# Kernel optimization log

Hardware: AMD Instinct MI355X
Metric: run time of the kernel (lower is better)

## Reference

```python
import jax, jax.numpy as jnp
import numpy as np

D = 1024
F = 256
EPS = 1e-5


def layer_norm(x, g, b):
    mu = jnp.mean(x, axis=-1, keepdims=True)
    var = jnp.mean((x - mu) ** 2, axis=-1, keepdims=True)
    return (x - mu) * jax.lax.rsqrt(var + EPS) * g + b


def setup_inputs() -> dict:
    key = jax.random.key(0)
    ks = jax.random.split(key, 8)
    B, S = 4, 4096
    return {
        "bottom_up_input": jax.random.normal(ks[0], (B, S, D), dtype=jnp.float32),
        "top_down_prediction": jax.random.normal(ks[1], (B, S, D), dtype=jnp.float32),
        "W_spec": jax.random.normal(ks[2], (2 * F, D), dtype=jnp.float32) * 0.02,
        "log_decay": jnp.linspace(-3.0, -0.001, F, dtype=jnp.float32),
        "frequencies": jax.random.normal(ks[3], (F,), dtype=jnp.float32) * 0.1,
        "W_from": jax.random.normal(ks[4], (D, 2 * F), dtype=jnp.float32) * 0.02,
        "ln1_g": jnp.ones((D,), jnp.float32),
        "ln1_b": jnp.zeros((D,), jnp.float32),
        "W1": jax.random.normal(ks[5], (D, D), dtype=jnp.float32) * 0.02,
        "b1": jnp.zeros((D,), jnp.float32),
        "W2": jax.random.normal(ks[6], (D, D), dtype=jnp.float32) * 0.02,
        "b2": jnp.zeros((D,), jnp.float32),
        "ln2_g": jnp.ones((D,), jnp.float32),
        "ln2_b": jnp.zeros((D,), jnp.float32),
        "error_weight": jnp.asarray(0.1, jnp.float32),
    }


def spectral_conv(x, W_spec, log_decay, frequencies, W_from, ln1_g, ln1_b):
    # x: [B,S,D]
    x = layer_norm(x, ln1_g, ln1_b)
    B, S, _ = x.shape
    spectral = jnp.einsum('bsd,fd->bsf', x, W_spec)  # [B,S,2F]
    u = jax.lax.complex(spectral[..., :F], spectral[..., F:])  # [B,S,F] complex
    decay = jax.nn.sigmoid(log_decay)
    omega = jnp.tanh(frequencies) * 0.1  # dt = 1.0
    rot = jax.lax.complex(jnp.cos(omega), jnp.sin(omega))  # [F]
    A = (decay * rot).astype(jnp.complex64)  # [F]
    # kernel[t] = A^t * rot, built with cumprod as in the original
    ones = jnp.ones((1, F), dtype=A.dtype)
    A_seq = jnp.broadcast_to(A[None, :], (S - 1, F))
    powers = jnp.cumprod(jnp.concatenate([ones, A_seq], axis=0), axis=0)  # [S,F]
    kernel = (powers * rot[None, :])[None]  # [1,S,F]
    n_fft = 2 * S
    U_f = jnp.fft.fft(u, n=n_fft, axis=1)
    K_f = jnp.fft.fft(kernel, n=n_fft, axis=1)
    y = jnp.fft.ifft(U_f * K_f, n=n_fft, axis=1)[:, :S, :]  # [B,S,F]
    spectral_out = jnp.concatenate([y.real, y.imag], axis=-1)  # [B,S,2F]
    return jnp.einsum('bsf,df->bsd', spectral_out, W_from)


def reference(bottom_up_input, top_down_prediction, W_spec, log_decay, frequencies,
              W_from, ln1_g, ln1_b, W1, b1, W2, b2, ln2_g, ln2_b, error_weight):
    bu_repr = spectral_conv(bottom_up_input, W_spec, log_decay, frequencies,
                            W_from, ln1_g, ln1_b)
    error = jnp.clip(bu_repr - top_down_prediction, -1.0, 1.0)
    corrected = bu_repr - jax.nn.sigmoid(error_weight) * error
    prediction_error = jnp.clip(jnp.mean(error ** 2), 0.0, 1.0)
    h = jax.nn.gelu(jnp.einsum('bsd,ed->bse', corrected, W1) + b1, approximate=False)
    h = jnp.einsum('bsd,ed->bse', h, W2) + b2
    next_prediction = layer_norm(h, ln2_g, ln2_b)
    return corrected, next_prediction, prediction_error
```

## Files before the change

kernel.cpp:

```cpp
#include <hip/hip_runtime.h>
#include <math.h>

#define Dn 1024
#define Fn 256
#define Sn 4096
#define Bn 4
#define Mn (Bn*Sn)
#define CHn 256
#define NCn (Sn/CHn)

typedef __bf16 bf16x8 __attribute__((ext_vector_type(8)));
typedef float  f32x4  __attribute__((ext_vector_type(4)));

__device__ inline unsigned short f2bf(float f) {
  unsigned int u = __float_as_uint(f);
  u += 0x7fffu + ((u >> 16) & 1u);
  return (unsigned short)(u >> 16);
}
__device__ inline float bf2f(unsigned short s) {
  return __uint_as_float(((unsigned int)s) << 16);
}

__device__ inline void async16(const void* g, void* l) {
  __builtin_amdgcn_global_load_lds(
      (__attribute__((address_space(1))) void*)(g),
      (__attribute__((address_space(3))) void*)(l), 16, 0, 0);
}

#define WAITVM(n) __builtin_amdgcn_s_waitcnt(0xF70 | (n))
#define BARRIER() asm volatile("s_barrier" ::: "memory")

__global__ __launch_bounds__(256) void convert_weights(
    const float* __restrict__ wspec, const float* __restrict__ wfrom,
    const float* __restrict__ w1, const float* __restrict__ w2,
    unsigned short* __restrict__ o_spec, unsigned short* __restrict__ o_from,
    unsigned short* __restrict__ o_w1, unsigned short* __restrict__ o_w2) {
  int i = blockIdx.x * 256 + threadIdx.x;
  if (i < 524288) {
    o_spec[i] = f2bf(wspec[i]);
    o_from[i] = f2bf(wfrom[i]);
  }
  o_w1[i] = f2bf(w1[i]);
  o_w2[i] = f2bf(w2[i]);
}

template <int IN_BF16, int OUT_BF16>
__global__ __launch_bounds__(256) void ln_kernel(
    const void* __restrict__ xin, const float* __restrict__ g,
    const float* __restrict__ b, void* __restrict__ out) {
  int row = blockIdx.x, tid = threadIdx.x;
  int wid = tid >> 6, lane = tid & 63;
  float4 v;
  if (IN_BF16) {
    ushort4 u = ((const ushort4*)xin)[(size_t)row * 256 + tid];
    v.x = bf2f(u.x); v.y = bf2f(u.y); v.z = bf2f(u.z); v.w = bf2f(u.w);
  } else {
    v = ((const float4*)xin)[(size_t)row * 256 + tid];
  }
  float s  = v.x + v.y + v.z + v.w;
  float ss = v.x * v.x + v.y * v.y + v.z * v.z + v.w * v.w;
  #pragma unroll
  for (int o = 32; o; o >>= 1) {
    s  += __shfl_down(s, o);
    ss += __shfl_down(ss, o);
  }
  __shared__ float r1[4], r2[4];
  if (lane == 0) { r1[wid] = s; r2[wid] = ss; }
  __syncthreads();
  s  = r1[0] + r1[1] + r1[2] + r1[3];
  ss = r2[0] + r2[1] + r2[2] + r2[3];
  float mu  = s * (1.0f / Dn);
  float var = ss * (1.0f / Dn) - mu * mu;
  float rs  = rsqrtf(var + 1e-5f);
  float4 gv = ((const float4*)g)[tid];
  float4 bv = ((const float4*)b)[tid];
  float o0 = (v.x - mu) * rs * gv.x + bv.x;
  float o1 = (v.y - mu) * rs * gv.y + bv.y;
  float o2 = (v.z - mu) * rs * gv.z + bv.z;
  float o3 = (v.w - mu) * rs * gv.w + bv.w;
  if (OUT_BF16) {
    ushort4 w;
    w.x = f2bf(o0); w.y = f2bf(o1); w.z = f2bf(o2); w.w = f2bf(o3);
    ((ushort4*)out)[(size_t)row * 256 + tid] = w;
  } else {
    float4 w; w.x = o0; w.y = o1; w.z = o2; w.w = o3;
    ((float4*)out)[(size_t)row * 256 + tid] = w;
  }
}

template <int MODE>
__global__ __launch_bounds__(256, 4) void gemm_bt(
    const unsigned short* __restrict__ A, const unsigned short* __restrict__ Bw,
    int K, int N,
    float* __restrict__ outF, unsigned short* __restrict__ outH,
    const float* __restrict__ td, const float* __restrict__ bias,
    const float* __restrict__ ew, float* __restrict__ errAcc) {
  __shared__ unsigned short As[2 * 4096];
  __shared__ unsigned short Bs[2 * 4096];
  __shared__ float red[4];

  int tid = threadIdx.x;
  int wid = tid >> 6, lane = tid & 63;
  int wm = wid >> 1, wn = wid & 1;
  int quad = lane >> 4, l16 = lane & 15;

  int g = blockIdx.x + gridDim.x * blockIdx.y;
  int nbn = gridDim.x;
  int gh = g >> 3;
  int bn = gh % nbn;
  int bm = (g & 7) + (gh / nbn) * 8;

  int r_lo = lane >> 2;
  int c8   = (lane & 3) * 8;

  const unsigned short* Abase = A + (size_t)bm * 128 * K;
  const unsigned short* Bbase = Bw + (size_t)bn * 128 * K;

  f32x4 acc[4][4] = {};

  const int T = K >> 5;
  auto issue = [&](int t, int stg) {
    int k0 = t << 5;
    #pragma unroll
    for (int s = 0; s < 2; ++s) {
      int chunk = s * 4 + wid;
      int r = chunk * 16 + r_lo;
      async16(Abase + (size_t)r * K + k0 + c8, As + stg * 4096 + chunk * 512);
      async16(Bbase + (size_t)r * K + k0 + c8, Bs + stg * 4096 + chunk * 512);
    }
  };

  issue(0, 0);

  for (int k = 0; k < T; ++k) {
    WAITVM(0);
    BARRIER();
    if (k + 1 < T) issue(k + 1, (k + 1) & 1);

    const unsigned short* Ab = As + (k & 1) * 4096;
    const unsigned short* Bb = Bs + (k & 1) * 4096;
    bf16x8 af[4], bf[4];
    #pragma unroll
    for (int i = 0; i < 4; i++)
      af[i] = *(const bf16x8*)(Ab + (wm * 64 + i * 16 + l16) * 32 + quad * 8);
    #pragma unroll
    for (int j = 0; j < 4; j++)
      bf[j] = *(const bf16x8*)(Bb + (wn * 64 + j * 16 + l16) * 32 + quad * 8);
    #pragma unroll
    for (int i = 0; i < 4; i++)
      #pragma unroll
      for (int j = 0; j < 4; j++)
        acc[i][j] = __builtin_amdgcn_mfma_f32_16x16x32_bf16(af[i], bf[j], acc[i][j], 0, 0, 0);
  }

  float esum = 0.0f;
  float sigw = 0.0f;
  if (MODE == 1) sigw = 1.0f / (1.0f + expf(-ew[0]));

  #pragma unroll
  for (int i = 0; i < 4; i++) {
    int row_base = bm * 128 + wm * 64 + i * 16 + quad * 4;
    #pragma unroll
    for (int j = 0; j < 4; j++) {
      int col = bn * 128 + wn * 64 + j * 16 + l16;
      #pragma unroll
      for (int r = 0; r < 4; r++) {
        size_t idx = (size_t)(row_base + r) * N + col;
        float v = acc[i][j][r];
        if (MODE == 0) {
          outH[idx] = f2bf(v);
        } else if (MODE == 1) {
          float e = v - td[idx];
          e = fminf(fmaxf(e, -1.0f), 1.0f);
          float corr = v - sigw * e;
          outF[idx] = corr;
          outH[idx] = f2bf(corr);
          esum += e * e;
        } else if (MODE == 2) {
          float h = v + bias[col];
          float gel = 0.5f * h * (1.0f + erff(h * 0.70710678118654752f));
          outH[idx] = f2bf(gel);
        } else if (MODE == 3) {
          outF[idx] = v + bias[col];
        } else {
          outH[idx] = f2bf(v + bias[col]);
        }
      }
    }
  }

  if (MODE == 1) {
    #pragma unroll
    for (int o = 32; o; o >>= 1) esum += __shfl_down(esum, o);
    if (lane == 0) red[wid] = esum;
    __syncthreads();
    if (tid == 0) atomicAdd(errAcc, red[0] + red[1] + red[2] + red[3]);
  }
}

__global__ __launch_bounds__(256) void scan_partial(
    const unsigned short* __restrict__ spec, const float* __restrict__ log_decay,
    const float* __restrict__ freq, float2* __restrict__ chunkfin) {
  int f = threadIdx.x;
  int bx = blockIdx.x;
  int b = bx / NCn, c = bx % NCn;
  float dec = 1.0f / (1.0f + expf(-log_decay[f]));
  float om  = tanhf(freq[f]) * 0.1f;
  float Are = dec * cosf(om), Aim = dec * sinf(om);
  const unsigned short* u = spec + ((size_t)b * Sn + (size_t)c * CHn) * 512 + f;
  float sre = 0.0f, sim = 0.0f;
  for (int t = 0; t < CHn; t++) {
    float ure = bf2f(u[(size_t)t * 512]);
    float uim = bf2f(u[(size_t)t * 512 + 256]);
    float nre = Are * sre - Aim * sim + ure;
    float nim = Are * sim + Aim * sre + uim;
    sre = nre; sim = nim;
  }
  chunkfin[(size_t)bx * 256 + f] = make_float2(sre, sim);
}

__global__ __launch_bounds__(256) void scan_carry(
    const float* __restrict__ log_decay, const float* __restrict__ freq,
    const float2* __restrict__ chunkfin, float2* __restrict__ carries) {
  int f = threadIdx.x;
  int b = blockIdx.x;
  float dec = 1.0f / (1.0f + expf(-log_decay[f]));
  float om  = tanhf(freq[f]) * 0.1f;
  float pre = dec * cosf(om), pim = dec * sinf(om);
  #pragma unroll
  for (int i = 0; i < 8; i++) {
    float nr = pre * pre - pim * pim;
    float ni = 2.0f * pre * pim;
    pre = nr; pim = ni;
  }
  float sre = 0.0f, sim = 0.0f;
  for (int c = 0; c < NCn; c++) {
    carries[(size_t)(b * NCn + c) * 256 + f] = make_float2(sre, sim);
    float2 cf = chunkfin[(size_t)(b * NCn + c) * 256 + f];
    float nre = pre * sre - pim * sim + cf.x;
    float nim = pre * sim + pim * sre + cf.y;
    sre = nre; sim = nim;
  }
}

__global__ __launch_bounds__(256) void scan_final(
    const unsigned short* __restrict__ spec, const float* __restrict__ log_decay,
    const float* __restrict__ freq, const float2* __restrict__ carries,
    unsigned short* __restrict__ outH) {
  int f = threadIdx.x;
  int bx = blockIdx.x;
  int b = bx / NCn, c = bx % NCn;
  float dec = 1.0f / (1.0f + expf(-log_decay[f]));
  float om  = tanhf(freq[f]) * 0.1f;
  float Are = dec * cosf(om), Aim = dec * sinf(om);
  float Rre = cosf(om), Rim = sinf(om);
  float2 s0 = carries[(size_t)bx * 256 + f];
  float sre = s0.x, sim = s0.y;
  const unsigned short* u = spec + ((size_t)b * Sn + (size_t)c * CHn) * 512 + f;
  unsigned short* o = outH + ((size_t)b * Sn + (size_t)c * CHn) * 512 + f;
  for (int t = 0; t < CHn; t++) {
    float ure = bf2f(u[(size_t)t * 512]);
    float uim = bf2f(u[(size_t)t * 512 + 256]);
    float nre = Are * sre - Aim * sim + ure;
    float nim = Are * sim + Aim * sre + uim;
    sre = nre; sim = nim;
    o[(size_t)t * 512]       = f2bf(Rre * sre - Rim * sim);
    o[(size_t)t * 512 + 256] = f2bf(Rre * sim + Rim * sre);
  }
}

__global__ void finalize_err(const float* __restrict__ errAcc, float* __restrict__ out) {
  float m = errAcc[0] * (1.0f / 16777216.0f);
  out[0] = fminf(fmaxf(m, 0.0f), 1.0f);
}

extern "C" void kernel_launch(void* const* d_in, const int* in_sizes, int n_in,
                              void* d_out, int out_size, void* d_ws, size_t ws_size,
                              hipStream_t stream) {
  (void)in_sizes; (void)n_in; (void)out_size; (void)ws_size;
  const float* x     = (const float*)d_in[0];
  const float* td    = (const float*)d_in[1];
  const float* wspec = (const float*)d_in[2];
  const float* logd  = (const float*)d_in[3];
  const float* freq  = (const float*)d_in[4];
  const float* wfrom = (const float*)d_in[5];
  const float* g1    = (const float*)d_in[6];
  const float* b1ln  = (const float*)d_in[7];
  const float* W1    = (const float*)d_in[8];
  const float* b1    = (const float*)d_in[9];
  const float* W2    = (const float*)d_in[10];
  const float* b2    = (const float*)d_in[11];
  const float* g2    = (const float*)d_in[12];
  const float* b2ln  = (const float*)d_in[13];
  const float* ew    = (const float*)d_in[14];

  char* ws = (char*)d_ws;
  size_t off = 0;
  float* errAcc = (float*)(ws + off);              off += 256;
  unsigned short* wspec_h = (unsigned short*)(ws + off); off += (size_t)512 * 1024 * 2;
  unsigned short* wfrom_h = (unsigned short*)(ws + off); off += (size_t)1024 * 512 * 2;
  unsigned short* w1_h    = (unsigned short*)(ws + off); off += (size_t)1024 * 1024 * 2;
  unsigned short* w2_h    = (unsigned short*)(ws + off); off += (size_t)1024 * 1024 * 2;
  unsigned short* xn_h   = (unsigned short*)(ws + off);
  unsigned short* corr_h = (unsigned short*)(ws + off);
  unsigned short* h2_h   = (unsigned short*)(ws + off); off += (size_t)Mn * 1024 * 2;
  unsigned short* spec  = (unsigned short*)(ws + off);
  unsigned short* h1_h  = (unsigned short*)(ws + off);  off += (size_t)Mn * 1024 * 2;
  unsigned short* so_h = (unsigned short*)(ws + off);  off += (size_t)Mn * 512 * 2;
  float2* chunkfin = (float2*)(ws + off);              off += (size_t)Bn * NCn * 256 * 8;
  float2* carries  = (float2*)(ws + off);              off += (size_t)Bn * NCn * 256 * 8;

  float* outCorr = (float*)d_out;
  float* outNP   = outCorr + (size_t)Mn * 1024;
  float* outErr  = outNP + (size_t)Mn * 1024;

  hipMemsetAsync(errAcc, 0, 4, stream);
  convert_weights<<<4096, 256, 0, stream>>>(wspec, wfrom, W1, W2,
                                            wspec_h, wfrom_h, w1_h, w2_h);
  ln_kernel<0, 1><<<Mn, 256, 0, stream>>>(x, g1, b1ln, xn_h);
  gemm_bt<0><<<dim3(512 / 128, Mn / 128), 256, 0, stream>>>(
      xn_h, wspec_h, 1024, 512, nullptr, spec, nullptr, nullptr, nullptr, nullptr);
  scan_partial<<<Bn * NCn, 256, 0, stream>>>(spec, logd, freq, chunkfin);
  scan_carry<<<Bn, 256, 0, stream>>>(logd, freq, chunkfin, carries);
  scan_final<<<Bn * NCn, 256, 0, stream>>>(spec, logd, freq, carries, so_h);
  gemm_bt<1><<<dim3(1024 / 128, Mn / 128), 256, 0, stream>>>(
      so_h, wfrom_h, 512, 1024, outCorr, corr_h, td, nullptr, ew, errAcc);
  gemm_bt<2><<<dim3(1024 / 128, Mn / 128), 256, 0, stream>>>(
      corr_h, w1_h, 1024, 1024, nullptr, h1_h, nullptr, b1, nullptr, nullptr);
  gemm_bt<4><<<dim3(1024 / 128, Mn / 128), 256, 0, stream>>>(
      h1_h, w2_h, 1024, 1024, nullptr, h2_h, nullptr, b2, nullptr, nullptr);
  ln_kernel<1, 0><<<Mn, 256, 0, stream>>>(h2_h, g2, b2ln, outNP);
  finalize_err<<<1, 1, 0, stream>>>(errAcc, outErr);
}
```

Baseline: 479.7 us.

## Add 256x256-tile 8-wave GEMM for large matmuls and shrink scan chunks

After: 465.4 us. 3.0% less time.

```diff
diff --git a/kernel.cpp b/kernel.cpp
--- a/kernel.cpp
+++ b/kernel.cpp
@@ -6,7 +6,7 @@
 #define Sn 4096
 #define Bn 4
 #define Mn (Bn*Sn)
-#define CHn 256
+#define CHn 64
 #define NCn (Sn/CHn)
 
 typedef __bf16 bf16x8 __attribute__((ext_vector_type(8)));
@@ -198,6 +198,161 @@
   }
 }
 
+template <int MODE, int NBN>
+__global__ __launch_bounds__(512, 2) void gemm256(
+    const unsigned short* __restrict__ A, const unsigned short* __restrict__ Bw,
+    int K,
+    float* __restrict__ outF, unsigned short* __restrict__ outH,
+    const float* __restrict__ td, const float* __restrict__ bias,
+    const float* __restrict__ ew, float* __restrict__ errAcc) {
+  __shared__ unsigned short As[2 * 16384];
+  __shared__ unsigned short Bs[2 * 16384];
+  __shared__ float red[8];
+
+  const int tid = threadIdx.x;
+  const int w = tid >> 6, l = tid & 63;
+  const int wm = w >> 2, wn = w & 3;
+  const int quad = l >> 4, l16 = l & 15;
+  const int sw = l16 & 7;
+  const int N = NBN * 256;
+
+  int g = blockIdx.x;
+  int gh = g >> 3;
+  int bn = gh % NBN;
+  int bm = (g & 7) + (gh / NBN) * 8;
+
+  const int r8 = w * 8 + (l >> 3);
+  const int gcol = ((l & 7) ^ (l >> 3)) * 8;
+  const unsigned short* Ag = A + (size_t)(bm * 256 + r8) * K + gcol;
+  const unsigned short* Bg = Bw + (size_t)(bn * 256 + r8) * K + gcol;
+
+  auto stage = [&](int t, int c) {
+    const int k0 = t << 6;
+    #pragma unroll
+    for (int i = 0; i < 4; i++) {
+      async16(Ag + (size_t)(i * 64) * K + k0, As + c * 16384 + i * 4096 + w * 512);
+      async16(Bg + (size_t)(i * 64) * K + k0, Bs + c * 16384 + i * 4096 + w * 512);
+    }
+  };
+
+  f32x4 acc[8][4] = {};
+  const int NT = K >> 6;
+
+  stage(0, 0);
+  stage(1, 1);
+  WAITVM(8);
+  BARRIER();
+
+  for (int t = 0; t < NT; ++t) {
+    const int c = t & 1;
+    const unsigned short* Ab = As + c * 16384;
+    const unsigned short* Bb = Bs + c * 16384;
+    bf16x8 af[8], bfr[4];
+
+    #pragma unroll
+    for (int m = 0; m < 8; m++)
+      af[m] = *(const bf16x8*)(Ab + (wm * 128 + m * 16 + l16) * 64 + ((quad ^ sw) << 3));
+    #pragma unroll
+    for (int n = 0; n < 4; n++)
+      bfr[n] = *(const bf16x8*)(Bb + (wn * 64 + n * 16 + l16) * 64 + ((quad ^ sw) << 3));
+    BARRIER();
+    __builtin_amdgcn_s_setprio(1);
+    #pragma unroll
+    for (int m = 0; m < 8; m++) {
+      acc[m][0] = __builtin_amdgcn_mfma_f32_16x16x32_bf16(af[m], bfr[0], acc[m][0], 0, 0, 0);
+      acc[m][1] = __builtin_amdgcn_mfma_f32_16x16x32_bf16(af[m], bfr[1], acc[m][1], 0, 0, 0);
+    }
+    __builtin_amdgcn_s_setprio(0);
+    BARRIER();
+
+    __builtin_amdgcn_s_setprio(1);
+    #pragma unroll
+    for (int m = 0; m < 8; m++) {
+      acc[m][2] = __builtin_amdgcn_mfma_f32_16x16x32_bf16(af[m], bfr[2], acc[m][2], 0, 0, 0);
+      acc[m][3] = __builtin_amdgcn_mfma_f32_16x16x32_bf16(af[m], bfr[3], acc[m][3], 0, 0, 0);
+    }
+    __builtin_amdgcn_s_setprio(0);
+    BARRIER();
+
+    #pragma unroll
+    for (int m = 0; m < 8; m++)
+      af[m] = *(const bf16x8*)(Ab + (wm * 128 + m * 16 + l16) * 64 + (((4 + quad) ^ sw) << 3));
+    #pragma unroll
+    for (int n = 0; n < 4; n++)
+      bfr[n] = *(const bf16x8*)(Bb + (wn * 64 + n * 16 + l16) * 64 + (((4 + quad) ^ sw) << 3));
+    BARRIER();
+    __builtin_amdgcn_s_setprio(1);
+    #pragma unroll
+    for (int m = 0; m < 8; m++) {
+      acc[m][0] = __builtin_amdgcn_mfma_f32_16x16x32_bf16(af[m], bfr[0], acc[m][0], 0, 0, 0);
+      acc[m][1] = __builtin_amdgcn_mfma_f32_16x16x32_bf16(af[m], bfr[1], acc[m][1], 0, 0, 0);
+    }
+    __builtin_amdgcn_s_setprio(0);
+    BARRIER();
+
+    if (t + 2 < NT) { stage(t + 2, c); WAITVM(8); }
+    else            { WAITVM(0); }
+    BARRIER();
+    __builtin_amdgcn_s_setprio(1);
+    #pragma unroll
+    for (int m = 0; m < 8; m++) {
+      acc[m][2] = __builtin_amdgcn_mfma_f32_16x16x32_bf16(af[m], bfr[2], acc[m][2], 0, 0, 0);
+      acc[m][3] = __builtin_amdgcn_mfma_f32_16x16x32_bf16(af[m], bfr[3], acc[m][3], 0, 0, 0);
+    }
+    __builtin_amdgcn_s_setprio(0);
+    BARRIER();
+  }
+
+  float esum = 0.0f;
+  float sigw = 0.0f;
+  if (MODE == 1) sigw = 1.0f / (1.0f + expf(-ew[0]));
+
+  #pragma unroll
+  for (int m = 0; m < 8; m++) {
+    int row_base = bm * 256 + wm * 128 + m * 16 + quad * 4;
+    #pragma unroll
+    for (int n = 0; n < 4; n++) {
+      int col = bn * 256 + wn * 64 + n * 16 + l16;
+      #pragma unroll
+      for (int r = 0; r < 4; r++) {
+        size_t idx = (size_t)(row_base + r) * N + col;
+        float v = acc[m][n][r];
+        if (MODE == 0) {
+          outH[idx] = f2bf(v);
+        } else if (MODE == 1) {
+          float e = v - td[idx];
+          e = fminf(fmaxf(e, -1.0f), 1.0f);
+          float corr = v - sigw * e;
+          outF[idx] = corr;
+          outH[idx] = f2bf(corr);
+          esum += e * e;
+        } else if (MODE == 2) {
+          float h = v + bias[col];
+          float gel = 0.5f * h * (1.0f + erff(h * 0.70710678118654752f));
+          outH[idx] = f2bf(gel);
+        } else if (MODE == 3) {
+          outF[idx] = v + bias[col];
+        } else {
+          outH[idx] = f2bf(v + bias[col]);
+        }
+      }
+    }
+  }
+
+  if (MODE == 1) {
+    #pragma unroll
+    for (int o = 32; o; o >>= 1) esum += __shfl_down(esum, o);
+    if (l == 0) red[w] = esum;
+    __syncthreads();
+    if (tid == 0) {
+      float s = 0.0f;
+      #pragma unroll
+      for (int i = 0; i < 8; i++) s += red[i];
+      atomicAdd(errAcc, s);
+    }
+  }
+}
+
 __global__ __launch_bounds__(256) void scan_partial(
     const unsigned short* __restrict__ spec, const float* __restrict__ log_decay,
     const float* __restrict__ freq, float2* __restrict__ chunkfin) {
@@ -228,7 +383,7 @@
   float om  = tanhf(freq[f]) * 0.1f;
   float pre = dec * cosf(om), pim = dec * sinf(om);
   #pragma unroll
-  for (int i = 0; i < 8; i++) {
+  for (int i = 0; i < 6; i++) {
     float nr = pre * pre - pim * pim;
     float ni = 2.0f * pre * pim;
     pre = nr; pim = ni;
@@ -323,12 +478,12 @@
   scan_partial<<<Bn * NCn, 256, 0, stream>>>(spec, logd, freq, chunkfin);
   scan_carry<<<Bn, 256, 0, stream>>>(logd, freq, chunkfin, carries);
   scan_final<<<Bn * NCn, 256, 0, stream>>>(spec, logd, freq, carries, so_h);
-  gemm_bt<1><<<dim3(1024 / 128, Mn / 128), 256, 0, stream>>>(
-      so_h, wfrom_h, 512, 1024, outCorr, corr_h, td, nullptr, ew, errAcc);
-  gemm_bt<2><<<dim3(1024 / 128, Mn / 128), 256, 0, stream>>>(
-      corr_h, w1_h, 1024, 1024, nullptr, h1_h, nullptr, b1, nullptr, nullptr);
-  gemm_bt<4><<<dim3(1024 / 128, Mn / 128), 256, 0, stream>>>(
-      h1_h, w2_h, 1024, 1024, nullptr, h2_h, nullptr, b2, nullptr, nullptr);
+  gemm256<1, 4><<<256, 512, 0, stream>>>(
+      so_h, wfrom_h, 512, outCorr, corr_h, td, nullptr, ew, errAcc);
+  gemm256<2, 4><<<256, 512, 0, stream>>>(
+      corr_h, w1_h, 1024, nullptr, h1_h, nullptr, b1, nullptr, nullptr);
+  gemm256<4, 4><<<256, 512, 0, stream>>>(
+      h1_h, w2_h, 1024, nullptr, h2_h, nullptr, b2, nullptr, nullptr);
   ln_kernel<1, 0><<<Mn, 256, 0, stream>>>(h2_h, g2, b2ln, outNP);
   finalize_err<<<1, 1, 0, stream>>>(errAcc, outErr);
 }
```
